# Kernel optimization log

Hardware: AMD Instinct MI355X
Metric: run time of the kernel (lower is better)

The kernel has to match this reference:

```python
import jax, jax.numpy as jnp
import numpy as np

B, CIN, H, W = 8, 64, 128, 128
COUT, K = 64, 3
STRIDE, PAD, DIL, G = 1, 1, 1, 1
T = K * K
HO = (H + 2 * PAD - (DIL * (K - 1) + 1)) // STRIDE + 1
WO = (W + 2 * PAD - (DIL * (K - 1) + 1)) // STRIDE + 1


def setup_inputs() -> dict:
    key = jax.random.key(0)
    ks = jax.random.split(key, 5)
    x = jax.random.normal(ks[0], (B, CIN, H, W), jnp.float32)
    offset = jax.random.normal(ks[1], (B, 2 * G * T, HO, WO), jnp.float32)
    mask = jax.random.uniform(ks[2], (B, G * T, HO, WO), jnp.float32)
    weight = jax.random.normal(ks[3], (COUT, CIN, K, K), jnp.float32) * (1.0 / np.sqrt(CIN * T))
    bias = jnp.zeros((COUT,), jnp.float32)
    return {"x": x, "offset": offset, "mask": mask, "weight": weight, "bias": bias}


def _gather(img_f, idx):
    # img_f: [Cg, H*W], idx: [T, Ho, Wo] -> [Cg, T, Ho, Wo]
    return img_f[:, idx]


def _dcn(x, offset, mask, weight, bias):
    Bn, Cin, Hh, Ww = x.shape
    Cout = weight.shape[0]
    Cg = Cin // G
    # offset channels laid out as [G, T, (dy, dx)] per DCNv2 convention
    off = offset.reshape(Bn, G, T, 2, HO, WO)
    dy, dx = off[:, :, :, 0], off[:, :, :, 1]  # [B, G, T, Ho, Wo]
    ky, kx = jnp.meshgrid(jnp.arange(K), jnp.arange(K), indexing="ij")
    ky = (ky.reshape(T) * DIL).astype(jnp.float32)
    kx = (kx.reshape(T) * DIL).astype(jnp.float32)
    base_y = (jnp.arange(HO) * STRIDE - PAD).astype(jnp.float32)
    base_x = (jnp.arange(WO) * STRIDE - PAD).astype(jnp.float32)
    # absolute sampling coordinates per (batch, def-group, tap, out-row, out-col)
    py = dy + base_y[None, None, None, :, None] + ky[None, None, :, None, None]
    px = dx + base_x[None, None, None, None, :] + kx[None, None, :, None, None]
    y0 = jnp.floor(py)
    x0 = jnp.floor(px)
    imgf = x.reshape(Bn, G, Cg, Hh * Ww)
    gather = jax.vmap(jax.vmap(_gather))  # over B and G
    sampled = jnp.zeros((Bn, G, Cg, T, HO, WO), x.dtype)
    # bilinear interpolation with zero padding outside the image
    for oy, ox in ((y0, x0), (y0, x0 + 1.0), (y0 + 1.0, x0), (y0 + 1.0, x0 + 1.0)):
        wgt = (1.0 - jnp.abs(py - oy)) * (1.0 - jnp.abs(px - ox))
        valid = (oy >= 0) & (oy < Hh) & (ox >= 0) & (ox < Ww)
        yi = jnp.clip(oy, 0, Hh - 1).astype(jnp.int32)
        xi = jnp.clip(ox, 0, Ww - 1).astype(jnp.int32)
        vals = gather(imgf, yi * Ww + xi)  # [B, G, Cg, T, Ho, Wo]
        sampled = sampled + vals * (wgt * valid)[:, :, None]
    # modulation mask, then accumulate taps into output channels
    m = mask.reshape(Bn, G, T, HO, WO)
    sampled = sampled * m[:, :, None]
    wr = weight.reshape(Cout, G, Cg, T)
    out = jnp.einsum("bgctij,ogct->boij", sampled, wr) + bias[None, :, None, None]
    return out


def reference(x, offset, mask, weight, bias):
    return _dcn(x, offset, mask, weight, bias)
```

## Files before the change

### kernel.cpp

```cpp
#include <hip/hip_runtime.h>
#include <stdint.h>

#define Bn   8
#define CIN  64
#define Hh   128
#define Wh   128
#define COUT 64
#define Tt   9
#define HO   128
#define WO   128
#define HW   (HO * WO)

#define RH     17
#define RWC    25
#define RREC   (RH * RWC)
#define RSTR   144
#define HALO_Y 4
#define HALO_X 4

typedef _Float16 h16;
typedef __attribute__((ext_vector_type(2)))  _Float16 h2;
typedef __attribute__((ext_vector_type(8)))  _Float16 h8;
typedef __attribute__((ext_vector_type(16))) float    f16v;

__device__ h16 g_xT[(size_t)Bn * Hh * Wh * CIN];
__device__ h16 g_wh[Tt * 4 * 2 * 64 * 8];

__global__ __launch_bounds__(256) void prep(const float* __restrict__ x,
                                            const float* __restrict__ w) {
    if (blockIdx.x >= Bn * Hh) {
        int tid = (blockIdx.x - Bn * Hh) * 256 + threadIdx.x;
        int t   = tid >> 12;
        int rem = tid & 4095;
        int ks  = rem >> 10;
        int mt  = (rem >> 9) & 1;
        int ln  = (rem >> 3) & 63;
        int j   = rem & 7;
        int o   = mt * 32 + (ln & 31);
        int c   = ks * 16 + ((ln >> 5) << 3) + j;
        g_wh[tid] = (h16)w[(size_t)(o * 64 + c) * 9 + t];
        return;
    }
    int b = blockIdx.x >> 7;
    int y = blockIdx.x & 127;
    __shared__ uint32_t tile[64][65];

    const float* src = x + ((size_t)b * CIN) * (Hh * Wh) + (size_t)y * Wh;
    int t    = threadIdx.x;
    int xp   = t & 63;
    int csub = t >> 6;
    #pragma unroll
    for (int cc = 0; cc < 64; cc += 4) {
        int c = cc + csub;
        float2 v = *(const float2*)(src + (size_t)c * (Hh * Wh) + xp * 2);
        uint32_t h0 = (uint32_t)__builtin_bit_cast(uint16_t, (h16)v.x);
        uint32_t h1 = (uint32_t)__builtin_bit_cast(uint16_t, (h16)v.y);
        tile[c][xp] = h0 | (h1 << 16);
    }
    __syncthreads();

    uint32_t* dst = (uint32_t*)(g_xT + (((size_t)b * Hh + y) * Wh) * CIN);
    int d  = t & 31;
    int xo = t >> 5;
    #pragma unroll
    for (int it = 0; it < 16; ++it) {
        int xg = it * 8 + xo;
        uint32_t lo = tile[2 * d][xg >> 1];
        uint32_t hi = tile[2 * d + 1][xg >> 1];
        int sh = (xg & 1) * 16;
        uint32_t l0 = (lo >> sh) & 0xffffu;
        uint32_t h1 = (hi >> sh) & 0xffffu;
        dst[xg * 32 + d] = l0 | (h1 << 16);
    }
}

__global__ __launch_bounds__(256) void dcn_main(
        const float* __restrict__ offset, const float* __restrict__ mask,
        const float* __restrict__ bias, float* __restrict__ out) {
    __shared__ __align__(16) uint8_t sreg[RREC * RSTR];

    int blk  = blockIdx.x;
    int b    = blk & 7;
    int s    = blk >> 3;
    int ty   = s >> 3, tx = s & 7;
    int i0   = ty * 8, j0 = tx * 16;
    int lane = threadIdx.x & 63;
    int wave = threadIdx.x >> 6;
    int n    = lane & 31;
    int g    = lane >> 5;

    const h16* xb = g_xT + (size_t)b * (Hh * Wh * CIN);

    int i = i0 + 2 * wave + (n >> 4);
    int j = j0 + (n & 15);
    int p = (i << 7) + j;

    const float* offB = offset + (size_t)b * (2 * Tt * HW);
    const float* mskB = mask   + (size_t)b * (Tt * HW);
    float dyv[Tt], dxv[Tt], mmv[Tt];
    #pragma unroll
    for (int t = 0; t < Tt; ++t) {
        dyv[t] = offB[(2 * t) * HW + p];
        dxv[t] = offB[(2 * t + 1) * HW + p];
        mmv[t] = mskB[t * HW + p];
    }

    {
        const int base_y = i0 - HALO_Y, base_x = j0 - HALO_X;
        #pragma unroll
        for (int it = 0; it < 14; ++it) {
            int idx  = it * 256 + threadIdx.x;
            int rec  = idx >> 3;
            int quad = idx & 7;
            if (rec < RREC) {
                int ry = rec / RWC, rx = rec - ry * RWC;
                int gy = min(max(base_y + ry, 0), Hh - 1);
                int gx = min(max(base_x + rx, 0), Wh - 1);
                uint4 v = *(const uint4*)(xb + ((gy << 7) + gx) * 64 + quad * 8);
                *(uint4*)(sreg + rec * RSTR + quad * 16) = v;
            }
        }
    }
    __syncthreads();

    f16v acc[2] = {};

    #pragma unroll
    for (int t = 0; t < Tt; ++t) {
        const int ky = t / 3, kx = t % 3;
        float py = dyv[t] + (float)(i + ky - 1);
        float px = dxv[t] + (float)(j + kx - 1);
        float fy = floorf(py), fx = floorf(px);
        int   y0 = (int)fy,    x0 = (int)fx;
        float ly = py - fy,    lx = px - fx;
        float hy = 1.f - ly,   hx = 1.f - lx;

        bool vy0 = (y0 >= 0) && (y0 < Hh);
        bool vy1 = (y0 >= -1) && (y0 < Hh - 1);
        bool vx0 = (x0 >= 0) && (x0 < Wh);
        bool vx1 = (x0 >= -1) && (x0 < Wh - 1);
        float m = mmv[t];
        float w00 = (vy0 && vx0) ? hy * hx * m : 0.f;
        float w01 = (vy0 && vx1) ? hy * lx * m : 0.f;
        float w10 = (vy1 && vx0) ? ly * hx * m : 0.f;
        float w11 = (vy1 && vx1) ? ly * lx * m : 0.f;

        int ry = y0 - i0 + HALO_Y;
        int rx = x0 - j0 + HALO_X;
        bool intile = (ry >= 0) & (ry <= RH - 2) & (rx >= 0) & (rx <= RWC - 2);
        int ryc = min(max(ry, 0), RH - 2), rxc = min(max(rx, 0), RWC - 2);
        int pl00 = ryc * RWC + rxc;
        const uint8_t* cbase = sreg + pl00 * RSTR + g * 16;

        union U4 { uint4 v; h2 h[4]; };
        U4 c00[4], c01[4], c10[4], c11[4];
        #pragma unroll
        for (int ks = 0; ks < 4; ++ks) {
            c00[ks].v = *(const uint4*)(cbase + ks * 32);
            c01[ks].v = *(const uint4*)(cbase + RSTR + ks * 32);
            c10[ks].v = *(const uint4*)(cbase + RWC * RSTR + ks * 32);
            c11[ks].v = *(const uint4*)(cbase + (RWC + 1) * RSTR + ks * 32);
        }
        if (__any(!intile)) {
            if (!intile) {
                int y0c = min(max(y0, 0), Hh - 1), y1c = min(max(y0 + 1, 0), Hh - 1);
                int x0c = min(max(x0, 0), Wh - 1), x1c = min(max(x0 + 1, 0), Wh - 1);
                const h16* r0 = xb + (size_t)(y0c * Wh) * CIN;
                const h16* r1 = xb + (size_t)(y1c * Wh) * CIN;
                #pragma unroll
                for (int ks = 0; ks < 4; ++ks) {
                    int c = ks * 16 + g * 8;
                    c00[ks].v = *(const uint4*)(r0 + x0c * CIN + c);
                    c01[ks].v = *(const uint4*)(r0 + x1c * CIN + c);
                    c10[ks].v = *(const uint4*)(r1 + x0c * CIN + c);
                    c11[ks].v = *(const uint4*)(r1 + x1c * CIN + c);
                }
            }
        }

        h2 W00 = {(h16)w00, (h16)w00};
        h2 W01 = {(h16)w01, (h16)w01};
        h2 W10 = {(h16)w10, (h16)w10};
        h2 W11 = {(h16)w11, (h16)w11};

        const h16* wt = g_wh + t * 4096;
        #pragma unroll
        for (int ks = 0; ks < 4; ++ks) {
            union { h2 r[4]; h8 v; } pk;
            #pragma unroll
            for (int e = 0; e < 4; ++e) {
                h2 r = c00[ks].h[e] * W00;
                r = c01[ks].h[e] * W01 + r;
                r = c10[ks].h[e] * W10 + r;
                r = c11[ks].h[e] * W11 + r;
                pk.r[e] = r;
            }
            #pragma unroll
            for (int mt = 0; mt < 2; ++mt) {
                h8 a = *(const h8*)(wt + (ks * 2 + mt) * 512 + lane * 8);
                acc[mt] = __builtin_amdgcn_mfma_f32_32x32x16_f16(
                    a, pk.v, acc[mt], 0, 0, 0);
            }
        }
    }

    #pragma unroll
    for (int mt = 0; mt < 2; ++mt) {
        #pragma unroll
        for (int r = 0; r < 16; ++r) {
            int o = mt * 32 + (r & 3) + 8 * (r >> 2) + 4 * g;
            out[(size_t)(b * COUT + o) * HW + p] = acc[mt][r] + bias[o];
        }
    }
}

extern "C" void kernel_launch(void* const* d_in, const int* in_sizes, int n_in,
                              void* d_out, int out_size, void* d_ws, size_t ws_size,
                              hipStream_t stream) {
    const float* x      = (const float*)d_in[0];
    const float* offset = (const float*)d_in[1];
    const float* mask   = (const float*)d_in[2];
    const float* weight = (const float*)d_in[3];
    const float* bias   = (const float*)d_in[4];
    (void)d_ws; (void)ws_size;

    prep<<<Bn * Hh + 144, 256, 0, stream>>>(x, weight);
    dcn_main<<<Bn * 128, 256, 0, stream>>>(offset, mask, bias, (float*)d_out);
}
```

Before: 121.8 us.

## Shrink LDS halo tile, add occupancy hint, stream corner loads per k-slice

```diff
diff --git a/kernel.cpp b/kernel.cpp
--- a/kernel.cpp
+++ b/kernel.cpp
@@ -11,12 +11,12 @@
 #define WO   128
 #define HW   (HO * WO)
 
-#define RH     17
-#define RWC    25
+#define RH     15
+#define RWC    23
 #define RREC   (RH * RWC)
 #define RSTR   144
-#define HALO_Y 4
-#define HALO_X 4
+#define HALO_Y 3
+#define HALO_X 3
 
 typedef _Float16 h16;
 typedef __attribute__((ext_vector_type(2)))  _Float16 h2;
@@ -74,7 +74,7 @@
     }
 }
 
-__global__ __launch_bounds__(256) void dcn_main(
+__global__ __launch_bounds__(256, 3) void dcn_main(
         const float* __restrict__ offset, const float* __restrict__ mask,
         const float* __restrict__ bias, float* __restrict__ out) {
     __shared__ __align__(16) uint8_t sreg[RREC * RSTR];
@@ -108,7 +108,7 @@
     {
         const int base_y = i0 - HALO_Y, base_x = j0 - HALO_X;
         #pragma unroll
-        for (int it = 0; it < 14; ++it) {
+        for (int it = 0; it < 11; ++it) {
             int idx  = it * 256 + threadIdx.x;
             int rec  = idx >> 3;
             int quad = idx & 7;
@@ -152,30 +152,17 @@
         int pl00 = ryc * RWC + rxc;
         const uint8_t* cbase = sreg + pl00 * RSTR + g * 16;
 
-        union U4 { uint4 v; h2 h[4]; };
-        U4 c00[4], c01[4], c10[4], c11[4];
-        #pragma unroll
-        for (int ks = 0; ks < 4; ++ks) {
-            c00[ks].v = *(const uint4*)(cbase + ks * 32);
-            c01[ks].v = *(const uint4*)(cbase + RSTR + ks * 32);
-            c10[ks].v = *(const uint4*)(cbase + RWC * RSTR + ks * 32);
-            c11[ks].v = *(const uint4*)(cbase + (RWC + 1) * RSTR + ks * 32);
-        }
-        if (__any(!intile)) {
-            if (!intile) {
-                int y0c = min(max(y0, 0), Hh - 1), y1c = min(max(y0 + 1, 0), Hh - 1);
-                int x0c = min(max(x0, 0), Wh - 1), x1c = min(max(x0 + 1, 0), Wh - 1);
-                const h16* r0 = xb + (size_t)(y0c * Wh) * CIN;
-                const h16* r1 = xb + (size_t)(y1c * Wh) * CIN;
-                #pragma unroll
-                for (int ks = 0; ks < 4; ++ks) {
-                    int c = ks * 16 + g * 8;
-                    c00[ks].v = *(const uint4*)(r0 + x0c * CIN + c);
-                    c01[ks].v = *(const uint4*)(r0 + x1c * CIN + c);
-                    c10[ks].v = *(const uint4*)(r1 + x0c * CIN + c);
-                    c11[ks].v = *(const uint4*)(r1 + x1c * CIN + c);
-                }
-            }
+        bool fb_any = __any(!intile);
+        const h16 *f00 = nullptr, *f01 = nullptr, *f10 = nullptr, *f11 = nullptr;
+        if (fb_any) {
+            int y0c = min(max(y0, 0), Hh - 1), y1c = min(max(y0 + 1, 0), Hh - 1);
+            int x0c = min(max(x0, 0), Wh - 1), x1c = min(max(x0 + 1, 0), Wh - 1);
+            const h16* r0 = xb + (size_t)(y0c * Wh) * CIN;
+            const h16* r1 = xb + (size_t)(y1c * Wh) * CIN;
+            f00 = r0 + x0c * CIN + g * 8;
+            f01 = r0 + x1c * CIN + g * 8;
+            f10 = r1 + x0c * CIN + g * 8;
+            f11 = r1 + x1c * CIN + g * 8;
         }
 
         h2 W00 = {(h16)w00, (h16)w00};
@@ -184,15 +171,30 @@
         h2 W11 = {(h16)w11, (h16)w11};
 
         const h16* wt = g_wh + t * 4096;
+        union U4 { uint4 v; h2 h[4]; };
         #pragma unroll
         for (int ks = 0; ks < 4; ++ks) {
+            U4 c00, c01, c10, c11;
+            const uint8_t* cb = cbase + ks * 32;
+            c00.v = *(const uint4*)(cb);
+            c01.v = *(const uint4*)(cb + RSTR);
+            c10.v = *(const uint4*)(cb + RWC * RSTR);
+            c11.v = *(const uint4*)(cb + (RWC + 1) * RSTR);
+            if (fb_any) {
+                if (!intile) {
+                    c00.v = *(const uint4*)(f00 + ks * 16);
+                    c01.v = *(const uint4*)(f01 + ks * 16);
+                    c10.v = *(const uint4*)(f10 + ks * 16);
+                    c11.v = *(const uint4*)(f11 + ks * 16);
+                }
+            }
             union { h2 r[4]; h8 v; } pk;
             #pragma unroll
             for (int e = 0; e < 4; ++e) {
-                h2 r = c00[ks].h[e] * W00;
-                r = c01[ks].h[e] * W01 + r;
-                r = c10[ks].h[e] * W10 + r;
-                r = c11[ks].h[e] * W11 + r;
+                h2 r = c00.h[e] * W00;
+                r = c01.h[e] * W01 + r;
+                r = c10.h[e] * W10 + r;
+                r = c11.h[e] * W11 + r;
                 pk.r[e] = r;
             }
             #pragma unroll
```

After: 127.9 us. 1.05x slower.
